# Performance work log

Hardware: AMD Instinct MI355X
Metric: run time of the kernel (lower is better)

The kernel has to match this reference:

```python
import jax, jax.numpy as jnp
import numpy as np

N_IN = 8
H1 = 128
H2 = 128


def _lin_init(key, out_d, in_d, bias=True):
    # torch nn.Linear default init: U(-1/sqrt(fan_in), 1/sqrt(fan_in))
    bound = 1.0 / np.sqrt(in_d)
    k1, k2 = jax.random.split(key)
    w = jax.random.uniform(k1, (out_d, in_d), minval=-bound, maxval=bound, dtype=jnp.float32)
    if bias:
        b = jax.random.uniform(k2, (out_d,), minval=-bound, maxval=bound, dtype=jnp.float32)
        return w, b
    return w


def setup_inputs() -> dict:
    key = jax.random.key(0)
    ks = jax.random.split(key, 9)
    T = jax.random.normal(ks[0], (65536, N_IN), dtype=jnp.float32)
    l = jax.random.normal(ks[1], (65536, N_IN), dtype=jnp.float32)
    l1_dot = jax.random.normal(ks[2], (65536, N_IN), dtype=jnp.float32)
    center = jax.random.normal(ks[3], (512, N_IN), dtype=jnp.float32)
    w1_1, b1_1 = _lin_init(ks[4], H1, N_IN)          # layer1 of SKIP layer
    w2_1, b2_1 = _lin_init(ks[5], H1, N_IN)          # layer2 of SKIP layer (takes x)
    w1_2, b1_2 = _lin_init(ks[6], H2, H1)            # layer1 of MUL layer
    w2_2, b2_2 = _lin_init(ks[7], H2, H1)            # layer2 of MUL layer
    w_out = _lin_init(ks[8], 1, H2, bias=False)      # final Linear, no bias
    return dict(T=T, l=l, l1_dot=l1_dot, center=center,
                w1_1=w1_1, b1_1=b1_1, w2_1=w2_1, b2_1=b2_1,
                w1_2=w1_2, b1_2=b1_2, w2_2=w2_2, b2_2=b2_2, w_out=w_out)


def _net_out(x, w1_1, b1_1, w2_1, b2_1, w1_2, b1_2, w2_2, b2_2, w_out):
    z1 = x @ w1_1.T + b1_1
    z2 = x @ w2_1.T + b2_1
    y = z1 * z2
    # layer 2: MUL -> y = (W1 y + b1) * (W2 y + b2)
    z1 = y @ w1_2.T + b1_2
    z2 = y @ w2_2.T + b2_2
    y = z1 * z2
    return y @ w_out.T  # (b, 1)


def _grad_term(x, xdot, w1_1, b1_1, w2_1, b2_1, w1_2, b1_2, w2_2, b2_2, w_out):
    # Faithful manual forward-mode Jacobian chain. torch's
    # matmul(diag_embed(z), W) == z[:, :, None] * W (same math, no (b,h,h) tensor).
    z1 = x @ w1_1.T + b1_1
    z2 = x @ w2_1.T + b2_1
    y = z1 * z2
    # initial jacobian is identity (b, n, n); SKIP update:
    # J = diag(z1) @ W2 + diag(z2) @ W1 @ I -> (b, H1, n)
    J = z1[:, :, None] * w2_1[None, :, :] + z2[:, :, None] * w1_1[None, :, :]
    # MUL layer: J = (diag(z1) @ W2 + diag(z2) @ W1) @ J
    z1 = y @ w1_2.T + b1_2
    z2 = y @ w2_2.T + b2_2
    J = (z1[:, :, None] * jnp.einsum('oh,bhn->bon', w2_2, J)
         + z2[:, :, None] * jnp.einsum('oh,bhn->bon', w1_2, J))  # (b, H2, n)
    J = jnp.einsum('oh,bhn->bon', w_out, J)  # (b, 1, n)
    return jnp.sum(J[:, 0, :] * xdot, axis=1)  # (b,)


def reference(T, l, l1_dot, center,
              w1_1, b1_1, w2_1, b2_1, w1_2, b1_2, w2_2, b2_2, w_out):
    args = (w1_1, b1_1, w2_1, b2_1, w1_2, b1_2, w2_2, b2_2, w_out)
    v_t = _net_out(T, *args)
    v_y = _net_out(l, *args)
    v_grad = _grad_term(l, l1_dot, *args)
    v_center = _net_out(center, *args)
    return (v_t, v_y, v_grad, v_center)
```

## Files before the change

### kernel.cpp

```cpp
#include <hip/hip_runtime.h>
#include <hip/hip_bf16.h>


#define NIN 8
#define H 128
#define BLK 256

typedef short short8 __attribute__((ext_vector_type(8)));
typedef float f32x4 __attribute__((ext_vector_type(4)));

__device__ __forceinline__ unsigned bf16_bits(float f) {
    unsigned u = __float_as_uint(f);
    return (u + 0x7fffu + ((u >> 16) & 1u)) >> 16;
}
__device__ __forceinline__ unsigned pack_bf16(float a, float b) {
    return bf16_bits(a) | (bf16_bits(b) << 16);
}
__device__ __forceinline__ short8 pack8(float4 a, float4 b) {
    uint4 u = make_uint4(pack_bf16(a.x, a.y), pack_bf16(a.z, a.w),
                         pack_bf16(b.x, b.y), pack_bf16(b.z, b.w));
    return __builtin_bit_cast(short8, u);
}

__global__ __launch_bounds__(256, 1) void conv_w(
    const float* __restrict__ W12, const float* __restrict__ W22,
    const float* __restrict__ W11, const float* __restrict__ W21,
    unsigned* __restrict__ ws)
{
    int i = blockIdx.x * 256 + threadIdx.x;
    const float2* a = reinterpret_cast<const float2*>(W12);
    const float2* b = reinterpret_cast<const float2*>(W22);
    float2 fa = a[i], fb = b[i];
    ws[i]        = pack_bf16(fa.x, fa.y);
    ws[8192 + i] = pack_bf16(fb.x, fb.y);
    if (i < 512) {
        int ot = i >> 6, lane = i & 63;
        int q = lane >> 4, c = lane & 15;
        int o = 16 * ot + c;
        uint4 f1 = make_uint4(0, 0, 0, 0), f2 = make_uint4(0, 0, 0, 0);
        if (q == 0) {
            const float4* r1 = reinterpret_cast<const float4*>(W11 + o * NIN);
            const float4* r2 = reinterpret_cast<const float4*>(W21 + o * NIN);
            float4 x0 = r1[0], x1 = r1[1];
            f1 = make_uint4(pack_bf16(x0.x, x0.y), pack_bf16(x0.z, x0.w),
                            pack_bf16(x1.x, x1.y), pack_bf16(x1.z, x1.w));
            float4 y0 = r2[0], y1 = r2[1];
            f2 = make_uint4(pack_bf16(y0.x, y0.y), pack_bf16(y0.z, y0.w),
                            pack_bf16(y1.x, y1.y), pack_bf16(y1.z, y1.w));
        }
        *reinterpret_cast<uint4*>(ws + 16384 + i * 4) = f1;
        *reinterpret_cast<uint4*>(ws + 18432 + i * 4) = f2;
    }
}

__global__ __launch_bounds__(BLK, 2) void net_kernel(
    const float* __restrict__ T, int nTb,
    const float* __restrict__ L, const float* __restrict__ Ld,
    const float* __restrict__ C, int nCb,
    const float* __restrict__ b11, const float* __restrict__ b21,
    const unsigned* __restrict__ wsb,
    const float* __restrict__ b12, const float* __restrict__ b22,
    const float* __restrict__ wout,
    float* __restrict__ outT, float* __restrict__ outY,
    float* __restrict__ outG, float* __restrict__ outC)
{
    alignas(16) __shared__ unsigned smem[16384];

    const int tid  = threadIdx.x;
    const int wave = tid >> 6;
    const int lane = tid & 63;
    const int q    = lane >> 4;
    const int c    = lane & 15;

    const int bid = blockIdx.x;
    const bool is_grad = (bid >= nCb + nTb);

    const unsigned* w12p = wsb;
    const unsigned* w22p = wsb + 8192;
    const unsigned* wf1p = wsb + 16384 + (lane << 2);
    const unsigned* wf2p = wsb + 18432 + (lane << 2);

    const short8 zf = {0, 0, 0, 0, 0, 0, 0, 0};

    if (!is_grad) {
        const float* X = (bid < nCb) ? C : T;
        float* o1      = (bid < nCb) ? outC : outT;
        const int sb   = ((bid < nCb) ? bid : (bid - nCb)) * BLK;
        const int wb   = 64 * wave;

        short8 xf[4];
#pragma unroll
        for (int st = 0; st < 4; ++st) {
            if (q == 0) {
                const float4* xp = reinterpret_cast<const float4*>(
                    X + (size_t)(sb + wb + 16 * st + c) * NIN);
                xf[st] = pack8(xp[0], xp[1]);
            } else xf[st] = zf;
        }

#pragma unroll 2
        for (int ot = 0; ot < 8; ++ot) {
            short8 wf1 = *reinterpret_cast<const short8*>(wf1p + ot * 256);
            short8 wf2 = *reinterpret_cast<const short8*>(wf2p + ot * 256);
            float4 bi1 = *reinterpret_cast<const float4*>(b11 + 16 * ot + 4 * q);
            float4 bi2 = *reinterpret_cast<const float4*>(b21 + 16 * ot + 4 * q);
            f32x4 c1 = {bi1.x, bi1.y, bi1.z, bi1.w};
            f32x4 c2 = {bi2.x, bi2.y, bi2.z, bi2.w};
#pragma unroll
            for (int st = 0; st < 4; ++st) {
                f32x4 z1 = __builtin_amdgcn_mfma_f32_16x16x32_bf16(wf1, xf[st], c1, 0, 0, 0);
                f32x4 z2 = __builtin_amdgcn_mfma_f32_16x16x32_bf16(wf2, xf[st], c2, 0, 0, 0);
                int srow = wb + 16 * st + c;
                int off  = (8 * ot + 2 * q) ^ ((srow & 7) << 2);
                *reinterpret_cast<uint2*>(&smem[srow * 64 + off]) =
                    make_uint2(pack_bf16(z1[0] * z2[0], z1[1] * z2[1]),
                               pack_bf16(z1[2] * z2[2], z1[3] * z2[3]));
            }
        }
        __syncthreads();

        short8 yf[4][4];
#pragma unroll
        for (int mt = 0; mt < 4; ++mt)
#pragma unroll
            for (int kt = 0; kt < 4; ++kt) {
                int row = wb + 16 * mt + c;
                yf[mt][kt] = *reinterpret_cast<const short8*>(
                    &smem[row * 64 + ((16 * kt + 4 * q) ^ ((row & 7) << 2))]);
            }

        f32x4 g[4] = {{0,0,0,0},{0,0,0,0},{0,0,0,0},{0,0,0,0}};
#pragma unroll 2
        for (int nt = 0; nt < 8; ++nt) {
            int oc = 16 * nt + c;
            short8 bf12[4], bf22[4];
#pragma unroll
            for (int kt = 0; kt < 4; ++kt) {
                int od = oc * 64 + 16 * kt + 4 * q;
                bf12[kt] = *reinterpret_cast<const short8*>(w12p + od);
                bf22[kt] = *reinterpret_cast<const short8*>(w22p + od);
            }
            float bb1 = b12[oc], bb2 = b22[oc], wvv = wout[oc];
#pragma unroll
            for (int mt = 0; mt < 4; ++mt) {
                f32x4 z1 = {bb1, bb1, bb1, bb1};
                f32x4 z2 = {bb2, bb2, bb2, bb2};
#pragma unroll
                for (int kt = 0; kt < 4; ++kt) {
                    z1 = __builtin_amdgcn_mfma_f32_16x16x32_bf16(yf[mt][kt], bf12[kt], z1, 0, 0, 0);
                    z2 = __builtin_amdgcn_mfma_f32_16x16x32_bf16(yf[mt][kt], bf22[kt], z2, 0, 0, 0);
                }
#pragma unroll
                for (int r = 0; r < 4; ++r)
                    g[mt][r] = fmaf(wvv, z1[r] * z2[r], g[mt][r]);
            }
        }
#pragma unroll
        for (int mt = 0; mt < 4; ++mt) {
            float rv[4];
#pragma unroll
            for (int r = 0; r < 4; ++r) {
                float v = g[mt][r];
                v += __shfl_xor(v, 1); v += __shfl_xor(v, 2);
                v += __shfl_xor(v, 4); v += __shfl_xor(v, 8);
                rv[r] = v;
            }
            if (c == 0) {
                int s = sb + wb + 16 * mt + 4 * q;
                *reinterpret_cast<float4*>(&o1[s]) = make_float4(rv[0], rv[1], rv[2], rv[3]);
            }
        }
    } else {
        const int sb = (bid - nCb - nTb) * (BLK / 2);
        const int wb = 32 * wave;

        short8 xf[2], xdf[2];
#pragma unroll
        for (int st = 0; st < 2; ++st) {
            if (q == 0) {
                size_t s = (size_t)(sb + wb + 16 * st + c) * NIN;
                const float4* xp = reinterpret_cast<const float4*>(L + s);
                const float4* dp = reinterpret_cast<const float4*>(Ld + s);
                xf[st]  = pack8(xp[0], xp[1]);
                xdf[st] = pack8(dp[0], dp[1]);
            } else { xf[st] = zf; xdf[st] = zf; }
        }

        const f32x4 zero4 = {0.f, 0.f, 0.f, 0.f};
#pragma unroll 2
        for (int ot = 0; ot < 8; ++ot) {
            short8 wf1 = *reinterpret_cast<const short8*>(wf1p + ot * 256);
            short8 wf2 = *reinterpret_cast<const short8*>(wf2p + ot * 256);
            float4 bi1 = *reinterpret_cast<const float4*>(b11 + 16 * ot + 4 * q);
            float4 bi2 = *reinterpret_cast<const float4*>(b21 + 16 * ot + 4 * q);
            f32x4 c1 = {bi1.x, bi1.y, bi1.z, bi1.w};
            f32x4 c2 = {bi2.x, bi2.y, bi2.z, bi2.w};
#pragma unroll
            for (int st = 0; st < 2; ++st) {
                f32x4 z1 = __builtin_amdgcn_mfma_f32_16x16x32_bf16(wf1, xf[st],  c1, 0, 0, 0);
                f32x4 z2 = __builtin_amdgcn_mfma_f32_16x16x32_bf16(wf2, xf[st],  c2, 0, 0, 0);
                f32x4 d1 = __builtin_amdgcn_mfma_f32_16x16x32_bf16(wf1, xdf[st], zero4, 0, 0, 0);
                f32x4 d2 = __builtin_amdgcn_mfma_f32_16x16x32_bf16(wf2, xdf[st], zero4, 0, 0, 0);
                int srow = wb + 16 * st + c;
                int off  = (8 * ot + 2 * q) ^ ((srow & 7) << 2);
                *reinterpret_cast<uint2*>(&smem[srow * 64 + off]) =
                    make_uint2(pack_bf16(z1[0] * z2[0], z1[1] * z2[1]),
                               pack_bf16(z1[2] * z2[2], z1[3] * z2[3]));
                float dy0 = d1[0] * z2[0] + z1[0] * d2[0];
                float dy1 = d1[1] * z2[1] + z1[1] * d2[1];
                float dy2 = d1[2] * z2[2] + z1[2] * d2[2];
                float dy3 = d1[3] * z2[3] + z1[3] * d2[3];
                *reinterpret_cast<uint2*>(&smem[(128 + srow) * 64 + off]) =
                    make_uint2(pack_bf16(dy0, dy1), pack_bf16(dy2, dy3));
            }
        }
        __syncthreads();

        short8 yf[2][4], df[2][4];
#pragma unroll
        for (int mt = 0; mt < 2; ++mt)
#pragma unroll
            for (int kt = 0; kt < 4; ++kt) {
                int row = wb + 16 * mt + c;
                int off = (16 * kt + 4 * q) ^ ((row & 7) << 2);
                yf[mt][kt] = *reinterpret_cast<const short8*>(&smem[row * 64 + off]);
                df[mt][kt] = *reinterpret_cast<const short8*>(&smem[(128 + row) * 64 + off]);
            }

        f32x4 gy[2] = {{0,0,0,0},{0,0,0,0}};
        f32x4 gg[2] = {{0,0,0,0},{0,0,0,0}};
#pragma unroll 2
        for (int nt = 0; nt < 8; ++nt) {
            int oc = 16 * nt + c;
            short8 bf12[4], bf22[4];
#pragma unroll
            for (int kt = 0; kt < 4; ++kt) {
                int od = oc * 64 + 16 * kt + 4 * q;
                bf12[kt] = *reinterpret_cast<const short8*>(w12p + od);
                bf22[kt] = *reinterpret_cast<const short8*>(w22p + od);
            }
            float bb1 = b12[oc], bb2 = b22[oc], wvv = wout[oc];
#pragma unroll
            for (int mt = 0; mt < 2; ++mt) {
                f32x4 z1 = {bb1, bb1, bb1, bb1};
                f32x4 z2 = {bb2, bb2, bb2, bb2};
                f32x4 d1 = {0, 0, 0, 0};
                f32x4 d2 = {0, 0, 0, 0};
#pragma unroll
                for (int kt = 0; kt < 4; ++kt) {
                    z1 = __builtin_amdgcn_mfma_f32_16x16x32_bf16(yf[mt][kt], bf12[kt], z1, 0, 0, 0);
                    z2 = __builtin_amdgcn_mfma_f32_16x16x32_bf16(yf[mt][kt], bf22[kt], z2, 0, 0, 0);
                    d1 = __builtin_amdgcn_mfma_f32_16x16x32_bf16(df[mt][kt], bf12[kt], d1, 0, 0, 0);
                    d2 = __builtin_amdgcn_mfma_f32_16x16x32_bf16(df[mt][kt], bf22[kt], d2, 0, 0, 0);
                }
#pragma unroll
                for (int r = 0; r < 4; ++r) {
                    gy[mt][r] = fmaf(wvv, z1[r] * z2[r], gy[mt][r]);
                    gg[mt][r] = fmaf(wvv, d1[r] * z2[r] + z1[r] * d2[r], gg[mt][r]);
                }
            }
        }
#pragma unroll
        for (int mt = 0; mt < 2; ++mt) {
            float ry[4], rg[4];
#pragma unroll
            for (int r = 0; r < 4; ++r) {
                float v = gy[mt][r];
                v += __shfl_xor(v, 1); v += __shfl_xor(v, 2);
                v += __shfl_xor(v, 4); v += __shfl_xor(v, 8);
                ry[r] = v;
                float w = gg[mt][r];
                w += __shfl_xor(w, 1); w += __shfl_xor(w, 2);
                w += __shfl_xor(w, 4); w += __shfl_xor(w, 8);
                rg[r] = w;
            }
            if (c == 0) {
                int s = sb + wb + 16 * mt + 4 * q;
                *reinterpret_cast<float4*>(&outY[s]) = make_float4(ry[0], ry[1], ry[2], ry[3]);
                *reinterpret_cast<float4*>(&outG[s]) = make_float4(rg[0], rg[1], rg[2], rg[3]);
            }
        }
    }
}

extern "C" void kernel_launch(void* const* d_in, const int* in_sizes, int n_in,
                              void* d_out, int out_size, void* d_ws, size_t ws_size,
                              hipStream_t stream) {
    const float* T      = (const float*)d_in[0];
    const float* l      = (const float*)d_in[1];
    const float* l1dot  = (const float*)d_in[2];
    const float* center = (const float*)d_in[3];
    const float* w11  = (const float*)d_in[4];
    const float* b11  = (const float*)d_in[5];
    const float* w21  = (const float*)d_in[6];
    const float* b21  = (const float*)d_in[7];
    const float* w12  = (const float*)d_in[8];
    const float* b12  = (const float*)d_in[9];
    const float* w22  = (const float*)d_in[10];
    const float* b22  = (const float*)d_in[11];
    const float* wout = (const float*)d_in[12];

    float* out = (float*)d_out;

    const int nT = in_sizes[0] / NIN;
    const int nL = in_sizes[1] / NIN;
    const int nC = in_sizes[3] / NIN;

    conv_w<<<32, 256, 0, stream>>>(w12, w22, w11, w21, (unsigned*)d_ws);

    const int nCb = nC / BLK;
    const int nTb = nT / BLK;
    const int nGb = nL / (BLK / 2);

    net_kernel<<<nCb + nTb + nGb, BLK, 0, stream>>>(
        T, nTb, l, l1dot, center, nCb,
        b11, b21,
        (const unsigned*)d_ws, b12, b22, wout,
        out,
        out + nT,
        out + nT + nL,
        out + nT + 2 * (size_t)nL);
}
```

Before: 120.5 us.

## Keep layer-1 activations in registers via permuted K layout, drop LDS round trip

Layer-1 MFMA outputs are now packed directly into the register fragments used as A operands of layer 2, instead of being written to shared memory and read back after a barrier. To make this work, the conv_w prep kernel permutes the K dimension of the layer-2 weights to match the register fragment ordering. This removes all LDS traffic and the __syncthreads. Launch bounds are raised to 4 blocks per SM. Fully unrolled loops and fragments held in registers may increase register pressure and conflict with the higher occupancy target.

```diff
diff --git a/kernel.cpp b/kernel.cpp
--- a/kernel.cpp
+++ b/kernel.cpp
@@ -8,6 +8,7 @@
 
 typedef short short8 __attribute__((ext_vector_type(8)));
 typedef float f32x4 __attribute__((ext_vector_type(4)));
+typedef unsigned uint32x4 __attribute__((ext_vector_type(4)));
 
 __device__ __forceinline__ unsigned bf16_bits(float f) {
     unsigned u = __float_as_uint(f);
@@ -28,17 +29,20 @@
     unsigned* __restrict__ ws)
 {
     int i = blockIdx.x * 256 + threadIdx.x;
-    const float2* a = reinterpret_cast<const float2*>(W12);
-    const float2* b = reinterpret_cast<const float2*>(W22);
-    float2 fa = a[i], fb = b[i];
-    ws[i]        = pack_bf16(fa.x, fa.y);
-    ws[8192 + i] = pack_bf16(fb.x, fb.y);
+    int oc = i >> 6, rem = i & 63;
+    int kt = rem >> 4, q = (rem >> 2) & 3, d = rem & 3;
+    int base = (d < 2) ? (16 * kt + 4 * q + 2 * d)
+                       : (64 + 16 * kt + 4 * q + 2 * (d - 2));
+    const float* r12 = W12 + oc * H;
+    const float* r22 = W22 + oc * H;
+    ws[i]        = pack_bf16(r12[base], r12[base + 1]);
+    ws[8192 + i] = pack_bf16(r22[base], r22[base + 1]);
     if (i < 512) {
         int ot = i >> 6, lane = i & 63;
-        int q = lane >> 4, c = lane & 15;
+        int qq = lane >> 4, c = lane & 15;
         int o = 16 * ot + c;
         uint4 f1 = make_uint4(0, 0, 0, 0), f2 = make_uint4(0, 0, 0, 0);
-        if (q == 0) {
+        if (qq == 0) {
             const float4* r1 = reinterpret_cast<const float4*>(W11 + o * NIN);
             const float4* r2 = reinterpret_cast<const float4*>(W21 + o * NIN);
             float4 x0 = r1[0], x1 = r1[1];
@@ -53,7 +57,7 @@
     }
 }
 
-__global__ __launch_bounds__(BLK, 2) void net_kernel(
+__global__ __launch_bounds__(BLK, 4) void net_kernel(
     const float* __restrict__ T, int nTb,
     const float* __restrict__ L, const float* __restrict__ Ld,
     const float* __restrict__ C, int nCb,
@@ -64,8 +68,6 @@
     float* __restrict__ outT, float* __restrict__ outY,
     float* __restrict__ outG, float* __restrict__ outC)
 {
-    alignas(16) __shared__ unsigned smem[16384];
-
     const int tid  = threadIdx.x;
     const int wave = tid >> 6;
     const int lane = tid & 63;
@@ -98,7 +100,8 @@
             } else xf[st] = zf;
         }
 
-#pragma unroll 2
+        uint32x4 yf[4][4];
+#pragma unroll
         for (int ot = 0; ot < 8; ++ot) {
             short8 wf1 = *reinterpret_cast<const short8*>(wf1p + ot * 256);
             short8 wf2 = *reinterpret_cast<const short8*>(wf2p + ot * 256);
@@ -110,24 +113,12 @@
             for (int st = 0; st < 4; ++st) {
                 f32x4 z1 = __builtin_amdgcn_mfma_f32_16x16x32_bf16(wf1, xf[st], c1, 0, 0, 0);
                 f32x4 z2 = __builtin_amdgcn_mfma_f32_16x16x32_bf16(wf2, xf[st], c2, 0, 0, 0);
-                int srow = wb + 16 * st + c;
-                int off  = (8 * ot + 2 * q) ^ ((srow & 7) << 2);
-                *reinterpret_cast<uint2*>(&smem[srow * 64 + off]) =
-                    make_uint2(pack_bf16(z1[0] * z2[0], z1[1] * z2[1]),
-                               pack_bf16(z1[2] * z2[2], z1[3] * z2[3]));
-            }
-        }
-        __syncthreads();
-
-        short8 yf[4][4];
-#pragma unroll
-        for (int mt = 0; mt < 4; ++mt)
-#pragma unroll
-            for (int kt = 0; kt < 4; ++kt) {
-                int row = wb + 16 * mt + c;
-                yf[mt][kt] = *reinterpret_cast<const short8*>(
-                    &smem[row * 64 + ((16 * kt + 4 * q) ^ ((row & 7) << 2))]);
-            }
+                unsigned u0 = pack_bf16(z1[0] * z2[0], z1[1] * z2[1]);
+                unsigned u1 = pack_bf16(z1[2] * z2[2], z1[3] * z2[3]);
+                if (ot < 4) { yf[st][ot][0] = u0;     yf[st][ot][1] = u1; }
+                else        { yf[st][ot - 4][2] = u0; yf[st][ot - 4][3] = u1; }
+            }
+        }
 
         f32x4 g[4] = {{0,0,0,0},{0,0,0,0},{0,0,0,0},{0,0,0,0}};
 #pragma unroll 2
@@ -147,8 +138,9 @@
                 f32x4 z2 = {bb2, bb2, bb2, bb2};
 #pragma unroll
                 for (int kt = 0; kt < 4; ++kt) {
-                    z1 = __builtin_amdgcn_mfma_f32_16x16x32_bf16(yf[mt][kt], bf12[kt], z1, 0, 0, 0);
-                    z2 = __builtin_amdgcn_mfma_f32_16x16x32_bf16(yf[mt][kt], bf22[kt], z2, 0, 0, 0);
+                    short8 af = __builtin_bit_cast(short8, yf[mt][kt]);
+                    z1 = __builtin_amdgcn_mfma_f32_16x16x32_bf16(af, bf12[kt], z1, 0, 0, 0);
+                    z2 = __builtin_amdgcn_mfma_f32_16x16x32_bf16(af, bf22[kt], z2, 0, 0, 0);
                 }
 #pragma unroll
                 for (int r = 0; r < 4; ++r)
@@ -186,8 +178,9 @@
             } else { xf[st] = zf; xdf[st] = zf; }
         }
 
+        uint32x4 yf[2][4], df[2][4];
         const f32x4 zero4 = {0.f, 0.f, 0.f, 0.f};
-#pragma unroll 2
+#pragma unroll
         for (int ot = 0; ot < 8; ++ot) {
             short8 wf1 = *reinterpret_cast<const short8*>(wf1p + ot * 256);
             short8 wf2 = *reinterpret_cast<const short8*>(wf2p + ot * 256);
@@ -201,31 +194,21 @@
                 f32x4 z2 = __builtin_amdgcn_mfma_f32_16x16x32_bf16(wf2, xf[st],  c2, 0, 0, 0);
                 f32x4 d1 = __builtin_amdgcn_mfma_f32_16x16x32_bf16(wf1, xdf[st], zero4, 0, 0, 0);
                 f32x4 d2 = __builtin_amdgcn_mfma_f32_16x16x32_bf16(wf2, xdf[st], zero4, 0, 0, 0);
-                int srow = wb + 16 * st + c;
-                int off  = (8 * ot + 2 * q) ^ ((srow & 7) << 2);
-                *reinterpret_cast<uint2*>(&smem[srow * 64 + off]) =
-                    make_uint2(pack_bf16(z1[0] * z2[0], z1[1] * z2[1]),
-                               pack_bf16(z1[2] * z2[2], z1[3] * z2[3]));
-                float dy0 = d1[0] * z2[0] + z1[0] * d2[0];
-                float dy1 = d1[1] * z2[1] + z1[1] * d2[1];
-                float dy2 = d1[2] * z2[2] + z1[2] * d2[2];
-                float dy3 = d1[3] * z2[3] + z1[3] * d2[3];
-                *reinterpret_cast<uint2*>(&smem[(128 + srow) * 64 + off]) =
-                    make_uint2(pack_bf16(dy0, dy1), pack_bf16(dy2, dy3));
-            }
-        }
-        __syncthreads();
-
-        short8 yf[2][4], df[2][4];
-#pragma unroll
-        for (int mt = 0; mt < 2; ++mt)
-#pragma unroll
-            for (int kt = 0; kt < 4; ++kt) {
-                int row = wb + 16 * mt + c;
-                int off = (16 * kt + 4 * q) ^ ((row & 7) << 2);
-                yf[mt][kt] = *reinterpret_cast<const short8*>(&smem[row * 64 + off]);
-                df[mt][kt] = *reinterpret_cast<const short8*>(&smem[(128 + row) * 64 + off]);
-            }
+                unsigned u0 = pack_bf16(z1[0] * z2[0], z1[1] * z2[1]);
+                unsigned u1 = pack_bf16(z1[2] * z2[2], z1[3] * z2[3]);
+                unsigned v0 = pack_bf16(d1[0] * z2[0] + z1[0] * d2[0],
+                                        d1[1] * z2[1] + z1[1] * d2[1]);
+                unsigned v1 = pack_bf16(d1[2] * z2[2] + z1[2] * d2[2],
+                                        d1[3] * z2[3] + z1[3] * d2[3]);
+                if (ot < 4) {
+                    yf[st][ot][0] = u0; yf[st][ot][1] = u1;
+                    df[st][ot][0] = v0; df[st][ot][1] = v1;
+                } else {
+                    yf[st][ot - 4][2] = u0; yf[st][ot - 4][3] = u1;
+                    df[st][ot - 4][2] = v0; df[st][ot - 4][3] = v1;
+                }
+            }
+        }
 
         f32x4 gy[2] = {{0,0,0,0},{0,0,0,0}};
         f32x4 gg[2] = {{0,0,0,0},{0,0,0,0}};
@@ -248,10 +231,12 @@
                 f32x4 d2 = {0, 0, 0, 0};
 #pragma unroll
                 for (int kt = 0; kt < 4; ++kt) {
-                    z1 = __builtin_amdgcn_mfma_f32_16x16x32_bf16(yf[mt][kt], bf12[kt], z1, 0, 0, 0);
-                    z2 = __builtin_amdgcn_mfma_f32_16x16x32_bf16(yf[mt][kt], bf22[kt], z2, 0, 0, 0);
-                    d1 = __builtin_amdgcn_mfma_f32_16x16x32_bf16(df[mt][kt], bf12[kt], d1, 0, 0, 0);
-                    d2 = __builtin_amdgcn_mfma_f32_16x16x32_bf16(df[mt][kt], bf22[kt], d2, 0, 0, 0);
+                    short8 af = __builtin_bit_cast(short8, yf[mt][kt]);
+                    short8 ad = __builtin_bit_cast(short8, df[mt][kt]);
+                    z1 = __builtin_amdgcn_mfma_f32_16x16x32_bf16(af, bf12[kt], z1, 0, 0, 0);
+                    z2 = __builtin_amdgcn_mfma_f32_16x16x32_bf16(af, bf22[kt], z2, 0, 0, 0);
+                    d1 = __builtin_amdgcn_mfma_f32_16x16x32_bf16(ad, bf12[kt], d1, 0, 0, 0);
+                    d2 = __builtin_amdgcn_mfma_f32_16x16x32_bf16(ad, bf22[kt], d2, 0, 0, 0);
                 }
 #pragma unroll
                 for (int r = 0; r < 4; ++r) {
```

Result: slower. 166.5 us (+38.2%).
